# Kernel optimization log

Hardware: AMD Instinct MI355X
Metric: run time of the kernel (lower is better)

Reference implementation:

```python
import jax, jax.numpy as jnp
import numpy as np

NS = [65536, 16384, 4096, 1024, 256, 64]          # nodes per level (64 = 8 graphs x 8 dense voxels)
ES = [1048576, 262144, 65536, 16384, 4096]        # edges per level (avg degree 16)
INS = [1, 15, 23, 31, 39]
OUTS = [12, 20, 28, 36, 44]
K = 5                                             # kernel_size


def setup_inputs():
    keys = iter(jax.random.split(jax.random.key(0), 64))
    d = {'x': jax.random.normal(next(keys), (NS[0], 1), jnp.float32),
         'pos': jax.random.uniform(next(keys), (NS[0], 3), jnp.float32)}
    for l in range(5):
        n, e, ci, co = NS[l], ES[l], INS[l], OUTS[l]
        d[f'src{l}'] = jax.random.randint(next(keys), (e,), 0, n)
        d[f'dst{l}'] = jax.random.randint(next(keys), (e,), 0, n)
        d[f'eattr{l}'] = jax.random.normal(next(keys), (e, 3), jnp.float32)
        d[f'cluster{l}'] = jax.random.randint(next(keys), (n,), 0, NS[l + 1])
        d[f'w1_{l}'] = jax.random.normal(next(keys), (3, K), jnp.float32) * 0.5
        d[f'b1_{l}'] = jnp.zeros((K,), jnp.float32)
        d[f'w2_{l}'] = jax.random.normal(next(keys), (K, ci * co), jnp.float32) / np.float32(np.sqrt(K * ci))
        d[f'b2_{l}'] = jnp.zeros((ci * co,), jnp.float32)
        d[f'root_{l}'] = jax.random.normal(next(keys), (ci, co), jnp.float32) / np.float32(np.sqrt(ci))
        d[f'bias_{l}'] = jnp.zeros((co,), jnp.float32)
    d['fc_w'] = jax.random.normal(next(keys), (8 * 47, 10), jnp.float32) / np.float32(np.sqrt(8 * 47))
    d['fc_b'] = jnp.zeros((10,), jnp.float32)
    return d


def _conv(x, src, dst, eattr, w1, b1, w2, b2, root, bias, n):
    # edge-conditioned kernel: MLP(edge_attr) -> [E, ci, co]
    h = jnp.tanh(eattr @ w1 + b1)                                  # [E, K]
    We = (h @ w2 + b2).reshape(eattr.shape[0], x.shape[1], -1)     # [E, ci, co]
    msg = jnp.einsum('ei,eio->eo', x[src], We)                     # gather + per-edge matvec
    s = jax.ops.segment_sum(msg, dst, num_segments=n)
    cnt = jax.ops.segment_sum(jnp.ones((dst.shape[0], 1), x.dtype), dst, num_segments=n)
    agg = s / jnp.maximum(cnt, 1.0)                                # mean aggregation
    return agg + x @ root + bias, jnp.mean(jnp.square(We))


def _pool(x, pos, cluster, n_next):
    # sparse voxel max pool on features, mean on positions; pos concatenated to features
    xm = jax.ops.segment_max(x, cluster, num_segments=n_next)
    xm = jnp.where(jnp.isfinite(xm), xm, 0.0)                      # empty voxels -> 0
    ps = jax.ops.segment_sum(pos, cluster, num_segments=n_next)
    cnt = jax.ops.segment_sum(jnp.ones((pos.shape[0], 1), pos.dtype), cluster, num_segments=n_next)
    pm = ps / jnp.maximum(cnt, 1.0)
    return jnp.concatenate([xm, pm], axis=1), pm


def reference(x, pos, src0, dst0, eattr0, cluster0, w1_0, b1_0, w2_0, b2_0, root_0, bias_0,
              src1, dst1, eattr1, cluster1, w1_1, b1_1, w2_1, b2_1, root_1, bias_1,
              src2, dst2, eattr2, cluster2, w1_2, b1_2, w2_2, b2_2, root_2, bias_2,
              src3, dst3, eattr3, cluster3, w1_3, b1_3, w2_3, b2_3, root_3, bias_3,
              src4, dst4, eattr4, cluster4, w1_4, b1_4, w2_4, b2_4, root_4, bias_4,
              fc_w, fc_b):
    lv = [(src0, dst0, eattr0, cluster0, w1_0, b1_0, w2_0, b2_0, root_0, bias_0),
          (src1, dst1, eattr1, cluster1, w1_1, b1_1, w2_1, b2_1, root_1, bias_1),
          (src2, dst2, eattr2, cluster2, w1_2, b1_2, w2_2, b2_2, root_2, bias_2),
          (src3, dst3, eattr3, cluster3, w1_3, b1_3, w2_3, b2_3, root_3, bias_3),
          (src4, dst4, eattr4, cluster4, w1_4, b1_4, w2_4, b2_4, root_4, bias_4)]
    closs = jnp.float32(0.0)
    for l, (src, dst, ea, cl, w1, b1, w2, b2, rt, bs) in enumerate(lv):
        x, c = _conv(x, src, dst, ea, w1, b1, w2, b2, rt, bs, NS[l])
        closs = closs + c
        x, pos = _pool(x, pos, cl, NS[l + 1])
    feat = x.reshape(-1, 8 * 47)                                   # [B, 8*47]
    logits = feat @ fc_w + fc_b
    return jax.nn.log_softmax(logits, axis=1), closs
```

## Files before the change

kernel.cpp:

```cpp
#include <hip/hip_runtime.h>
#include <hip/hip_fp16.h>
#include <math.h>


#define NT0   512
#define TSZ0  2048
#define NBK0  256
#define CAP0  4608
#define NT1   128
#define TSZ1  2048
#define NBK1  256
#define CAP1  1280

__device__ __forceinline__ float ftanh(float x) {
    float e = __expf(2.f * x);
    return 1.f - 2.f / (e + 1.f);
}

__device__ __forceinline__ unsigned fenc(float f) {
    int b = __float_as_int(f);
    return (b < 0) ? ~(unsigned)b : ((unsigned)b | 0x80000000u);
}
__device__ __forceinline__ float fdec(unsigned u) {
    int b = (u & 0x80000000u) ? (int)(u & 0x7fffffffu) : ~(int)u;
    return __int_as_float(b);
}

__device__ __forceinline__ float row_val(const unsigned* __restrict__ row,
                                         int i, int CI) {
    float cn = __uint_as_float(row[CI]);
    if (i < CI - 3) return (cn == 0.f) ? 0.f : fdec(row[i]);
    return __uint_as_float(row[i]) / fmaxf(cn, 1.f);
}

struct Seg4 {
    const int* idx[4];
    int*       cnt[4];
    int*       rp [4];
    int*       out[4];
    int        n  [4];
    int        nb [4];
    int        tstart[5];
};

struct GA {
    const int *src0, *dst0; const float* ea0;
    const int *src1, *dst1; const float* ea1;
    const float *x0, *pos0;
    const int* cluster[5];
    const float *w1[5], *b1[5], *w2[5], *b2[5], *root[5], *bias[5];
    const int* srcE[3]; const float* eaE[3];
    const float *fc_w, *fc_b;
    int *bcnt, *bcnt1;
    float4 *pay2, *pay1, *rec1;
    float *y0, *xn0;
    unsigned* raw[5];
    float *H, *sq;
    int *bs1, *rp1;
    Seg4 sg;
    float* out;
    int hb0[4], hsB;
};

__global__ __launch_bounds__(256) void k1_fuseA(GA A)
{
    __shared__ float4 stg[TSZ0];
    __shared__ unsigned char bkb[TSZ0];
    __shared__ int hb_[256], gb_[256], ls_[256], cu_[256];

    int B = blockIdx.x, t = threadIdx.x;

    if (B < NT0) {
        hb_[t] = 0;
        __syncthreads();
        int base = B * TSZ0 + t;
        int dreg[8];
        #pragma unroll
        for (int k = 0; k < 8; k++) {
            dreg[k] = A.dst0[base + k * 256];
            atomicAdd(&hb_[dreg[k] >> 8], 1);
        }
        __syncthreads();
        int c = hb_[t];
        gb_[t] = c ? atomicAdd(&A.bcnt[t], c) : 0;
        ls_[t] = c;
        __syncthreads();
        for (int d = 1; d < 256; d <<= 1) {
            int u = (t >= d) ? ls_[t - d] : 0;
            __syncthreads();
            ls_[t] += u;
            __syncthreads();
        }
        int ex = ls_[t] - c;
        ls_[t] = ex;
        cu_[t] = ex;
        __syncthreads();

        float w1r[15], b1r[5];
        #pragma unroll
        for (int i = 0; i < 15; i++) w1r[i] = A.w1[0][i];
        #pragma unroll
        for (int i = 0; i < 5; i++)  b1r[i] = A.b1[0][i];
        float acc[20];
        #pragma unroll
        for (int i = 0; i < 20; i++) acc[i] = 0.f;
        #pragma unroll
        for (int k = 0; k < 8; k++) {
            int i = base + k * 256;
// ... 145 lines not shown
        for (int i = 0; i < 5; i++)  b1r[i] = b1p[i];
        float acc[20];
        #pragma unroll
        for (int i = 0; i < 20; i++) acc[i] = 0.f;
        int base = bloc * 256 * K + t;
        for (int it = 0; it < K; it++) {
            int e = base + it * 256;
            if (e < Ej) {
                float e0 = ea[e * 3], e1 = ea[e * 3 + 1], e2 = ea[e * 3 + 2];
                float h[5];
                #pragma unroll
                for (int q = 0; q < 5; q++)
                    h[q] = ftanh(e0 * w1r[q] + e1 * w1r[5 + q] + e2 * w1r[10 + q] + b1r[q]);
                int p = 5;
                #pragma unroll
                for (int q = 0; q < 5; q++) {
                    acc[q] += h[q];
                    #pragma unroll
                    for (int q2 = q; q2 < 5; q2++) acc[p++] += h[q] * h[q2];
                }
            }
        }
        float* red = (float*)hb_;
        int wid = t >> 6, lane = t & 63;
        #pragma unroll
        for (int v = 0; v < 20; v++) {
            float s = acc[v];
            #pragma unroll
            for (int o = 32; o; o >>= 1) s += __shfl_down(s, o);
            if (lane == 0) red[wid * 20 + v] = s;
        }
        __syncthreads();
        if (t < 20)
            atomicAdd(&A.H[(j + 2) * 20 + t],
                      red[t] + red[20 + t] + red[40 + t] + red[60 + t]);
        return;
    }
    B -= A.hsB;
    {
        int s = 0;
        while (s < 3 && B >= A.sg.tstart[s + 1]) s++;
        int i0 = (B - A.sg.tstart[s]) * 1024;
        const int* idx = A.sg.idx[s];
        int* cnt = A.sg.cnt[s];
        int n = A.sg.n[s];
        #pragma unroll
        for (int j = 0; j < 4; j++) {
            int i = i0 + j * 256 + t;
            if (i < n) atomicAdd(&cnt[idx[i]], 1);
        }
    }
}

__global__ __launch_bounds__(256) void k2_fuseB(GA A)
{
    __shared__ alignas(16) char poolc[34048];
    int B = blockIdx.x, t = threadIdx.x;

    if (B < NBK0) {
        float4* stg = (float4*)poolc;
        float*  Sx  = (float*)(poolc + 16384);
        unsigned char* key = (unsigned char*)(poolc + 23552);
        short* inv = (short*)(poolc + 24576);
        int* hist = (int*)(poolc + 26624);
        int* st   = (int*)(poolc + 27648);
        int* cur  = (int*)(poolc + 28672);
        float* wsm = (float*)(poolc + 29696);

        if (t < 60) wsm[t] = A.w2[0][t];
        else if (t >= 64  && t < 76)  wsm[60 + t - 64]  = A.b2[0][t - 64];
        else if (t >= 128 && t < 140) wsm[72 + t - 128] = A.root[0][t - 128];
        else if (t >= 192 && t < 204) wsm[84 + t - 192] = A.bias[0][t - 192];

        int n = A.bcnt[B];
        if (n > CAP0) n = CAP0;
        size_t base = (size_t)B * CAP0;
        float s0 = 0.f, s1 = 0.f, s2 = 0.f, s3 = 0.f, s4 = 0.f, s5 = 0.f, dg = 0.f;

        for (int c0 = 0; c0 < n; c0 += 1024) {
            int cn = min(1024, n - c0);
            hist[t] = 0;
            __syncthreads();
            #pragma unroll
            for (int k = 0; k < 4; k++) {
                int j = k * 256 + t;
                if (j < cn) {
                    float4 R = A.pay2[base + c0 + j];
                    stg[j] = R;
                    int rel = (int)(__float_as_uint(R.w) >> 16) & 255;
                    key[j] = (unsigned char)rel;
                    atomicAdd(&hist[rel], 1);
                }
            }
            __syncthreads();
            int h = hist[t];
            int acc = h;
            st[t] = acc;
            __syncthreads();
            for (int d = 1; d < 256; d <<= 1) {
                int u = (t >= d) ? st[t - d] : 0;
                __syncthreads();
                acc += u;
                st[t] = acc;
                __syncthreads();
            }
            int ex = acc - h;
            st[t] = ex;
            cur[t] = ex;
            __syncthreads();
            #pragma unroll
            for (int k = 0; k < 4; k++) {
                int j = k * 256 + t;
                if (j < cn) {
                    int p = atomicAdd(&cur[key[j]], 1);
                    inv[p] = (short)j;
                }
            }
            __syncthreads();
            for (int q = st[t]; q < cur[t]; q++) {
                float4 R = stg[inv[q]];
                union HU { float f; __half2 h2; } a01, a23;
                a01.f = R.y; a23.f = R.z;
                unsigned wbits = __float_as_uint(R.w);
                float xv = R.x;
                s0 += xv;
                s1 += __low2float(a01.h2)  * xv;
                s2 += __high2float(a01.h2) * xv;
                s3 += __low2float(a23.h2)  * xv;
                s4 += __high2float(a23.h2) * xv;
                s5 += __half2float(__ushort_as_half((unsigned short)(wbits & 0xffffu))) * xv;
                dg += 1.f;
            }
            __syncthreads();
        }
        Sx[t] = s0;        Sx[256 + t] = s1;  Sx[512 + t] = s2;
        Sx[768 + t] = s3;  Sx[1024 + t] = s4; Sx[1280 + t] = s5;
        Sx[1536 + t] = dg;
        __syncthreads();
        int v0 = B << 8;
        for (int u = t; u < 256 * 12; u += 256) {
            int rel = u / 12, o = u - rel * 12;
            float dgv = Sx[1536 + rel];
            float invd = 1.f / fmaxf(dgv, 1.f);
            float msg = wsm[60 + o] * Sx[rel] + wsm[o] * Sx[256 + rel] +
                        wsm[12 + o] * Sx[512 + rel] + wsm[24 + o] * Sx[768 + rel] +
                        wsm[36 + o] * Sx[1024 + rel] + wsm[48 + o] * Sx[1280 + rel];
            float xv = A.x0[v0 + rel];
            A.y0[(size_t)(v0 + rel) * 12 + o] =
                msg * invd + xv * wsm[72 + o] + wsm[84 + o];
        }
        return;
    }
    B -= NBK0;
    int* sc = (int*)poolc;
    if (B < 1) {
        int c = A.bcnt1[t];
        if (c > CAP1) c = CAP1;
        sc[t] = c;
        __syncthreads();
        for (int d = 1; d < 256; d <<= 1) {
            int u = (t >= d) ? sc[t - d] : 0;
            __syncthreads();
            sc[t] += u;
            __syncthreads();
        }
        A.bs1[t] = sc[t] - c;
        if (t == 255) { A.bs1[256] = sc[255]; A.rp1[16384] = sc[255]; }
        return;
    }
    B -= 1;
    if (B < 3) {
        int s = B;
        int nb = A.sg.nb[s];
        const int* cnt = A.sg.cnt[s];
        int* rp = A.sg.rp[s];
        int VPT = nb >> 8;
        int i0 = t * VPT;
        int sum = 0;
        for (int k = 0; k < VPT; k++) sum += cnt[i0 + k];
        int acc = sum;
        sc[t] = acc;
        __syncthreads();
        for (int d = 1; d < 256; d <<= 1) {
            int t2 = (t >= d) ? sc[t - d] : 0;
            __syncthreads();
            acc += t2;
            sc[t] = acc;
            __syncthreads();
        }
        int running = acc - sum;
        for (int k = 0; k < VPT; k++) {
            rp[i0 + k] = running;
            running += cnt[i0 + k];
        }
        if (t == 255) rp[nb] = running;
        return;
    }
    B -= 3;
    if (B < 1) {
        int* big = (int*)poolc;
        int* scx = (int*)(poolc + 32768);
        int* tot = (int*)(poolc + 33792);
        const int* cnt = A.sg.cnt[3];
        int* rp = A.sg.rp[3];
        int carry = 0;
        for (int p = 0; p < 2; p++) {
            if (p == 1) carry = tot[0];
// ... 48 lines not shown
            float w[5];
            #pragma unroll
            for (int k = 0; k < 5; k++) w[k] = w2l[k * cico + u];
            int p = 0;
            #pragma unroll
            for (int k = 0; k < 5; k++) {
                #pragma unroll
                for (int k2 = k; k2 < 5; k2++) d[p++] += w[k] * w[k2];
            }
            #pragma unroll
            for (int k = 0; k < 5; k++) d[15 + k] += b * w[k];
            d[20] += b * b;
        }
        #pragma unroll
        for (int i = 0; i < 21; i++) {
            #pragma unroll
            for (int off = 32; off; off >>= 1) d[i] += __shfl_down(d[i], off);
        }
        if (t == 0) {
            static const int EA[5] = {1048576, 262144, 65536, 16384, 4096};
            const float* H1 = A.H + l * 20;
            const float* H2 = H1 + 5;
            float sq = (float)EA[l] * d[20];
            #pragma unroll
            for (int k = 0; k < 5; k++) sq += 2.f * d[15 + k] * H1[k];
            int p = 0;
            #pragma unroll
            for (int k = 0; k < 5; k++) {
                #pragma unroll
                for (int k2 = k; k2 < 5; k2++) {
                    sq += ((k == k2) ? 1.f : 2.f) * d[p] * H2[p];
                    p++;
                }
            }
            A.sq[l] = sq;
        }
    }
}

__global__ __launch_bounds__(256) void k3_fuseC(GA A)
{
    __shared__ float4 st4[CAP1];
    __shared__ short  inv[CAP1];
    __shared__ int h64[64], l64[64], c64[64];
    int B = blockIdx.x, t = threadIdx.x;

    if (B < A.sg.tstart[4]) {
        int s = 0;
        while (s < 3 && B >= A.sg.tstart[s + 1]) s++;
        int i0 = (B - A.sg.tstart[s]) * 1024;
        const int* idx = A.sg.idx[s];
        int* cnt = A.sg.cnt[s];
        const int* rp = A.sg.rp[s];
        int* out = A.sg.out[s];
        int n = A.sg.n[s];
        #pragma unroll
        for (int j = 0; j < 4; j++) {
            int i = i0 + j * 256 + t;
            if (i < n) {
                int d = idx[i];
                int p = atomicSub(&cnt[d], 1) - 1;
                out[rp[d] + p] = i;
            }
        }
        return;
    }
    B -= A.sg.tstart[4];
    {
        int b = B;
        int n = A.bcnt1[b];
        if (n > CAP1) n = CAP1;
        size_t base = (size_t)b * CAP1;
        for (int j = t; j < n; j += 256) st4[j] = A.pay1[base + j];
        if (t < 64) h64[t] = 0;
        __syncthreads();
        for (int j = t; j < n; j += 256) {
            int rel = (int)(__float_as_uint(st4[j].x) >> 16) & 63;
            atomicAdd(&h64[rel], 1);
        }
        __syncthreads();
        if (t < 64) {
            int v = h64[t];
            int val = v;
            #pragma unroll
            for (int d = 1; d < 64; d <<= 1) {
                int u = __shfl_up(val, d);
                if (t >= d) val += u;
            }
            l64[t] = val - v;
            c64[t] = val - v;
        }
        __syncthreads();
        for (int j = t; j < n; j += 256) {
            int rel = (int)(__float_as_uint(st4[j].x) >> 16) & 63;
            int p = atomicAdd(&c64[rel], 1);
            inv[p] = (short)j;
        }
        __syncthreads();
        int lo = A.bs1[b];
        for (int j = t; j < n; j += 256)
            A.rec1[lo + j] = st4[inv[j]];
        if (t < 64) A.rp1[(b << 6) + t] = lo + l64[t];
    }
}

__global__ __launch_bounds__(256) void k4_pool0(GA A)
{
    int gt = blockIdx.x * 256 + threadIdx.x;
    if (gt >= 16384 * 15) return;
    int c = gt / 15, o = gt - c * 15;
    int r0 = A.sg.rp[3][c], r1 = A.sg.rp[3][c + 1];
    const int* cnid = A.sg.out[3];
    int d = r1 - r0;
    if (o < 12) {
        float m = -INFINITY;
        for (int j = r0; j < r1; j++)
            m = fmaxf(m, A.y0[(size_t)cnid[j] * 12 + o]);
        if (d == 0 || !isfinite(m)) m = 0.f;
        A.xn0[c * 15 + o] = m;
    } else {
        int k = o - 12;
        float sum = 0.f;
        for (int j = r0; j < r1; j++)
            sum += A.pos0[cnid[j] * 3 + k];
        A.xn0[c * 15 + o] = sum / fmaxf((float)d, 1.f);
    }
}

__global__ __launch_bounds__(256) void k5_conv1(GA A)
{
    constexpr int CI = 15, CO = 20, CH = 48, CICO = CI * CO, RN = 24;
    __shared__ float w1s[20];
    __shared__ float4 recb[CH];
    __shared__ int   svb[CH];
    __shared__ float hb[CH * 6];
    __shared__ float xs[CH * CI];
    __shared__ float Sx[6 * CI];
    __shared__ float xown[CI];

    int t = threadIdx.x, v = blockIdx.x;
    if (t < 20) w1s[t] = (t < 15) ? A.w1[1][t] : A.b1[1][t - 15];
    if (t < CI) xown[t] = A.xn0[v * CI + t];
    int r0 = A.rp1[v], r1 = A.rp1[v + 1];
    int d = r1 - r0;
    float acc = 0.f;

    for (int c0 = r0; c0 < r1; c0 += CH) {
        int cn = min(CH, r1 - c0);
        if (t < cn) {
            float4 R = A.rec1[c0 + t];
            recb[t] = R;
            svb[t]  = (int)(__float_as_uint(R.x) & 0xffffu);
            hb[t * 6] = 1.f;
        }
        __syncthreads();
        if (t < cn * 5) {
            int j = t / 5, k = t % 5;
            float e0 = recb[j].y, e1 = recb[j].z, e2 = recb[j].w;
            hb[j * 6 + 1 + k] =
                ftanh(e0 * w1s[k] + e1 * w1s[5 + k] + e2 * w1s[10 + k] + w1s[15 + k]);
        }
        for (int u = t; u < cn * CI; u += 256) {
            int j = u / CI, i = u - j * CI;
            xs[u] = A.xn0[svb[j] * CI + i];
        }
        __syncthreads();
        if (t < 6 * CI) {
            int i = t / 6, k6 = t - (t / 6) * 6;
            for (int j = 0; j < cn; j++)
                acc += hb[j * 6 + k6] * xs[j * CI + i];
        }
        __syncthreads();
    }

    if (t < 6 * CI) Sx[t] = acc;
    __syncthreads();

    if (t < CO) {
        float m = 0.f;
        const float* w2 = A.w2[1];
        const float* b2 = A.b2[1];
        for (int i = 0; i < CI; i++) {
            m += b2[i * CO + t] * Sx[i * 6];
            #pragma unroll
            for (int k = 0; k < 5; k++)
                m += w2[k * CICO + i * CO + t] * Sx[i * 6 + 1 + k];
        }
        m /= fmaxf((float)d, 1.f);
        for (int i = 0; i < CI; i++) m += xown[i] * A.root[1][i * CO + t];
        m += A.bias[1][t];
        int c = A.cluster[1][v];
        unsigned* orow = A.raw[1] + (size_t)c * RN;
        atomicMax(&orow[t], fenc(m));
        if (t < 3) atomicAdd((float*)&orow[CO + t], xown[CI - 3 + t]);
        if (t == 0) atomicAdd((float*)&orow[CO + 3], 1.f);
    }
}

template<int CI, int CO>
__global__ __launch_bounds__(256) void coopP_k(GA A, int l)
{
    constexpr int CH = 48, CICO = CI * CO, RL = CI + 1, RN = CO + 4;
    __shared__ float w1s[20];
    __shared__ int   eb[CH], svb[CH];
    __shared__ float hb[CH * 6];
    __shared__ float xs[CH * CI];
    __shared__ float Sx[6 * CI];
    __shared__ float xown[CI];

    int t = threadIdx.x, v = blockIdx.x;
    int s = l - 2;
    const unsigned* rin = A.raw[l - 1];
    const int* rp = A.sg.rp[s];
    const int* eid = A.sg.out[s];
    const int* src = A.srcE[s];
    const float* eattr = A.eaE[s];

    if (t < 20) w1s[t] = (t < 15) ? A.w1[l][t] : A.b1[l][t - 15];
    if (t < CI) xown[t] = row_val(rin + (size_t)v * RL, t, CI);
    int r0 = rp[v], r1 = rp[v + 1];
    int d = r1 - r0;
    float acc = 0.f;

    for (int c0 = r0; c0 < r1; c0 += CH) {
        int cn = min(CH, r1 - c0);
        if (t < cn) {
            int e = eid[c0 + t];
            eb[t]  = e;
            svb[t] = src[e];
            hb[t * 6] = 1.f;
        }
        __syncthreads();
        if (t < cn * 5) {
            int j = t / 5, k = t % 5;
            int e = eb[j];
            float e0 = eattr[e * 3], e1 = eattr[e * 3 + 1], e2 = eattr[e * 3 + 2];
            hb[j * 6 + 1 + k] =
                ftanh(e0 * w1s[k] + e1 * w1s[5 + k] + e2 * w1s[10 + k] + w1s[15 + k]);
        }
        for (int u = t; u < cn * CI; u += 256) {
            int j = u / CI, i = u - j * CI;
            xs[u] = row_val(rin + (size_t)svb[j] * RL, i, CI);
        }
        __syncthreads();
        if (t < 6 * CI) {
            int i = t / 6, k6 = t - (t / 6) * 6;
            for (int j = 0; j < cn; j++)
                acc += hb[j * 6 + k6] * xs[j * CI + i];
        }
        __syncthreads();
    }

    if (t < 6 * CI) Sx[t] = acc;
    __syncthreads();

    if (t < CO) {
        float m = 0.f;
        const float* w2 = A.w2[l];
        const float* b2 = A.b2[l];
        for (int i = 0; i < CI; i++) {
            m += b2[i * CO + t] * Sx[i * 6];
            #pragma unroll
            for (int k = 0; k < 5; k++)
                m += w2[k * CICO + i * CO + t] * Sx[i * 6 + 1 + k];
        }
        m /= fmaxf((float)d, 1.f);
        for (int i = 0; i < CI; i++) m += xown[i] * A.root[l][i * CO + t];
        m += A.bias[l][t];
        int c = A.cluster[l][v];
        unsigned* orow = A.raw[l] + (size_t)c * RN;
        atomicMax(&orow[t], fenc(m));
        if (t < 3) atomicAdd((float*)&orow[CO + t], xown[CI - 3 + t]);
        if (t == 0) atomicAdd((float*)&orow[CO + 3], 1.f);
    }
}

__global__ __launch_bounds__(128) void k9_fc(GA A)
{
    __shared__ float feat[8 * 376];
    __shared__ float logit[80];
    __shared__ float roff[8];
    const unsigned* r5 = A.raw[4];
    for (int idx = threadIdx.x; idx < 64 * 47; idx += 128) {
        int n = idx / 47, i = idx - n * 47;
        int b = n >> 3, s = n & 7;
        feat[b * 376 + s * 47 + i] = row_val(r5 + (size_t)n * 48, i, 47);
    }
    __syncthreads();
    int t = threadIdx.x;
    if (t < 80) {
        int b = t / 10, j = t % 10;
        float acc = A.fc_b[j];
        for (int k = 0; k < 376; k++) acc += feat[b * 376 + k] * A.fc_w[k * 10 + j];
        logit[t] = acc;
    }
    __syncthreads();
    if (t < 8) {
        float m = -1e30f;
        for (int j = 0; j < 10; j++) m = fmaxf(m, logit[t * 10 + j]);
        float ssum = 0.f;
        for (int j = 0; j < 10; j++) ssum += expf(logit[t * 10 + j] - m);
        roff[t] = m + logf(ssum);
    }
    __syncthreads();
    if (t < 80) A.out[t] = logit[t] - roff[t / 10];
    if (t == 0) {
        const float* sq = A.sq;
        float closs = 0.f;
        closs += sq[0] * (1.0f / 12582912.0f);
        closs += sq[1] * (1.0f / 78643200.0f);
        closs += sq[2] * (1.0f / 42205184.0f);
        closs += sq[3] * (1.0f / 18284544.0f);
        closs += sq[4] * (1.0f / 7028736.0f);
        A.out[80] = closs;
    }
}


extern "C" void kernel_launch(void* const* d_in, const int* in_sizes, int n_in,
                              void* d_out, int out_size, void* d_ws, size_t ws_size,
                              hipStream_t stream)
{
    static const int NSa[6] = {65536, 16384, 4096, 1024, 256, 64};
    static const int ESa[5] = {1048576, 262144, 65536, 16384, 4096};
    static const int RNa[5] = {16, 24, 32, 40, 48};

    int* wsw = (int*)d_ws;
    size_t off = 0;
    auto alw = [&](size_t n) -> size_t {
        size_t p = off; off += (n + 63) & ~(size_t)63; return p;
    };
    size_t degO[5];
    for (int l = 2; l < 5; l++) degO[l] = alw(NSa[l]);
    size_t cdeg0O = alw(NSa[1]);
    size_t HO    = alw(100);
    size_t bcO   = alw(NBK0);
    size_t bc1O  = alw(NBK1);
    size_t rawO[5];
    for (int l = 1; l < 5; l++) rawO[l] = alw((size_t)NSa[l + 1] * RNa[l]);
    size_t zeroWords = off;
    size_t rpO[5], eidO[5];
    for (int l = 2; l < 5; l++) rpO[l]  = alw(NSa[l] + 1);
    size_t crp0O = alw(NSa[1] + 1);
    for (int l = 2; l < 5; l++) eidO[l] = alw(ESa[l]);
    size_t cnid0O = alw(NSa[0]);
    size_t pay2O = alw((size_t)NBK0 * CAP0 * 4);
    size_t y0O   = alw((size_t)NSa[0] * 12);
    size_t xn0O  = alw((size_t)NSa[1] * 15);
    size_t bs1O  = alw(NBK1 + 1);
    size_t pay1O = alw((size_t)NBK1 * CAP1 * 4);
    size_t rec1O = alw((size_t)ESa[1] * 4);
    size_t rp1O  = alw(NSa[1] + 1);
    size_t sqO   = alw(8);

    GA A{};
    A.src0 = (const int*)d_in[2];  A.dst0 = (const int*)d_in[3];
    A.ea0  = (const float*)d_in[4];
    A.src1 = (const int*)d_in[12]; A.dst1 = (const int*)d_in[13];
    A.ea1  = (const float*)d_in[14];
    A.x0   = (const float*)d_in[0];
    A.pos0 = (const float*)d_in[1];
    for (int l = 0; l < 5; l++) {
        A.cluster[l] = (const int*)d_in[5 + 10 * l];
        A.w1[l]   = (const float*)d_in[6 + 10 * l];
        A.b1[l]   = (const float*)d_in[7 + 10 * l];
        A.w2[l]   = (const float*)d_in[8 + 10 * l];
        A.b2[l]   = (const float*)d_in[9 + 10 * l];
        A.root[l] = (const float*)d_in[10 + 10 * l];
        A.bias[l] = (const float*)d_in[11 + 10 * l];
    }
    for (int s = 0; s < 3; s++) {
        A.srcE[s] = (const int*)d_in[2 + 10 * (s + 2)];
        A.eaE[s]  = (const float*)d_in[4 + 10 * (s + 2)];
    }
    A.fc_w = (const float*)d_in[52];
    A.fc_b = (const float*)d_in[53];
    A.bcnt  = wsw + bcO;
    A.bcnt1 = wsw + bc1O;
    A.pay2 = (float4*)(wsw + pay2O);
    A.pay1 = (float4*)(wsw + pay1O);
    A.rec1 = (float4*)(wsw + rec1O);
    A.y0   = (float*)(wsw + y0O);
    A.xn0  = (float*)(wsw + xn0O);
    for (int l = 1; l < 5; l++) A.raw[l] = (unsigned*)(wsw + rawO[l]);
    A.H  = (float*)(wsw + HO);
    A.sq = (float*)(wsw + sqO);
    A.bs1 = wsw + bs1O;
    A.rp1 = wsw + rp1O;
    A.out = (float*)d_out;

    int tiles = 0;
    for (int s = 0; s < 3; s++) {
        int l = s + 2;
        A.sg.idx[s] = (const int*)d_in[3 + 10 * l];
        A.sg.cnt[s] = wsw + degO[l];
        A.sg.rp [s] = wsw + rpO[l];
        A.sg.out[s] = wsw + eidO[l];
        A.sg.n  [s] = ESa[l];
        A.sg.nb [s] = NSa[l];
        A.sg.tstart[s] = tiles;
        tiles += (ESa[l] + 1023) / 1024;
    }
    A.sg.idx[3] = (const int*)d_in[5];
    A.sg.cnt[3] = wsw + cdeg0O;
    A.sg.rp [3] = wsw + crp0O;
    A.sg.out[3] = wsw + cnid0O;
    A.sg.n  [3] = NSa[0];
    A.sg.nb [3] = NSa[1];
    A.sg.tstart[3] = tiles;
    tiles += (NSa[0] + 1023) / 1024;
    A.sg.tstart[4] = tiles;

    int hsB = 0;
    A.hb0[0] = 0;
    for (int j = 0; j < 3; j++) {
        hsB += (ESa[j + 2] + 2047) / 2048;
        A.hb0[j + 1] = hsB;
    }
    A.hsB = hsB;

    hipMemsetAsync(d_ws, 0, zeroWords * 4, stream);

    k1_fuseA<<<NT0 + NT1 + hsB + tiles, 256, 0, stream>>>(A);
    k2_fuseB<<<NBK0 + 1 + 3 + 1 + 5,    256, 0, stream>>>(A);
    k3_fuseC<<<tiles + NBK1,            256, 0, stream>>>(A);
    k4_pool0<<<(16384 * 15 + 255) / 256, 256, 0, stream>>>(A);
    k5_conv1<<<NSa[1],                  256, 0, stream>>>(A);
    coopP_k<23, 28><<<NSa[2],           256, 0, stream>>>(A, 2);
    coopP_k<31, 36><<<NSa[3],           256, 0, stream>>>(A, 3);
    coopP_k<39, 44><<<NSa[4],           256, 0, stream>>>(A, 4);
    k9_fc<<<1, 128, 0, stream>>>(A);
}
```

Measured before the change: 342.1 us.

## Write level-0 conv outputs in cluster-sorted order and shrink per-node conv blocks

Moves the level-0 conv out of the scan kernel into its own kernel that runs after the cluster counting sort. It writes y0 rows directly at each node's sorted cluster slot and stores positions in that same order, so the pooling kernel reads contiguous rows instead of gathering through a node-id list. It also cuts the per-node conv kernels for levels 1-4 from 256 to 64 threads, looping over the work, to reduce idle lanes. The cost is one extra launch and an extra positions copy.

```diff
diff --git a/kernel.cpp b/kernel.cpp
--- a/kernel.cpp
+++ b/kernel.cpp
@@ -54,6 +54,8 @@
     int *bcnt, *bcnt1;
     float4 *pay2, *pay1, *rec1;
     float *y0, *xn0;
+    int* rank0;
+    float* posp;
     unsigned* raw[5];
     float *H, *sq;
     int *bs1, *rp1;
@@ -305,107 +307,12 @@
     }
 }
 
-__global__ __launch_bounds__(256) void k2_fuseB(GA A)
+__global__ __launch_bounds__(256) void k2_scans(GA A)
 {
     __shared__ alignas(16) char poolc[34048];
     int B = blockIdx.x, t = threadIdx.x;
-
-    if (B < NBK0) {
-        float4* stg = (float4*)poolc;
-        float*  Sx  = (float*)(poolc + 16384);
-        unsigned char* key = (unsigned char*)(poolc + 23552);
-        short* inv = (short*)(poolc + 24576);
-        int* hist = (int*)(poolc + 26624);
-        int* st   = (int*)(poolc + 27648);
-        int* cur  = (int*)(poolc + 28672);
-        float* wsm = (float*)(poolc + 29696);
-
-        if (t < 60) wsm[t] = A.w2[0][t];
-        else if (t >= 64  && t < 76)  wsm[60 + t - 64]  = A.b2[0][t - 64];
-        else if (t >= 128 && t < 140) wsm[72 + t - 128] = A.root[0][t - 128];
-        else if (t >= 192 && t < 204) wsm[84 + t - 192] = A.bias[0][t - 192];
-
-        int n = A.bcnt[B];
-        if (n > CAP0) n = CAP0;
-        size_t base = (size_t)B * CAP0;
-        float s0 = 0.f, s1 = 0.f, s2 = 0.f, s3 = 0.f, s4 = 0.f, s5 = 0.f, dg = 0.f;
-
-        for (int c0 = 0; c0 < n; c0 += 1024) {
-            int cn = min(1024, n - c0);
-            hist[t] = 0;
-            __syncthreads();
-            #pragma unroll
-            for (int k = 0; k < 4; k++) {
-                int j = k * 256 + t;
-                if (j < cn) {
-                    float4 R = A.pay2[base + c0 + j];
-                    stg[j] = R;
-                    int rel = (int)(__float_as_uint(R.w) >> 16) & 255;
-                    key[j] = (unsigned char)rel;
-                    atomicAdd(&hist[rel], 1);
-                }
-            }
-            __syncthreads();
-            int h = hist[t];
-            int acc = h;
-            st[t] = acc;
-            __syncthreads();
-            for (int d = 1; d < 256; d <<= 1) {
-                int u = (t >= d) ? st[t - d] : 0;
-                __syncthreads();
-                acc += u;
-                st[t] = acc;
-                __syncthreads();
-            }
-            int ex = acc - h;
-            st[t] = ex;
-            cur[t] = ex;
-            __syncthreads();
-            #pragma unroll
-            for (int k = 0; k < 4; k++) {
-                int j = k * 256 + t;
-                if (j < cn) {
-                    int p = atomicAdd(&cur[key[j]], 1);
-                    inv[p] = (short)j;
-                }
-            }
-            __syncthreads();
-            for (int q = st[t]; q < cur[t]; q++) {
-                float4 R = stg[inv[q]];
-                union HU { float f; __half2 h2; } a01, a23;
-                a01.f = R.y; a23.f = R.z;
-                unsigned wbits = __float_as_uint(R.w);
-                float xv = R.x;
-                s0 += xv;
-                s1 += __low2float(a01.h2)  * xv;
-                s2 += __high2float(a01.h2) * xv;
-                s3 += __low2float(a23.h2)  * xv;
-                s4 += __high2float(a23.h2) * xv;
-                s5 += __half2float(__ushort_as_half((unsigned short)(wbits & 0xffffu))) * xv;
-                dg += 1.f;
-            }
-            __syncthreads();
-        }
-        Sx[t] = s0;        Sx[256 + t] = s1;  Sx[512 + t] = s2;
-        Sx[768 + t] = s3;  Sx[1024 + t] = s4; Sx[1280 + t] = s5;
-        Sx[1536 + t] = dg;
-        __syncthreads();
-        int v0 = B << 8;
-        for (int u = t; u < 256 * 12; u += 256) {
-            int rel = u / 12, o = u - rel * 12;
-            float dgv = Sx[1536 + rel];
-            float invd = 1.f / fmaxf(dgv, 1.f);
-            float msg = wsm[60 + o] * Sx[rel] + wsm[o] * Sx[256 + rel] +
-                        wsm[12 + o] * Sx[512 + rel] + wsm[24 + o] * Sx[768 + rel] +
-                        wsm[36 + o] * Sx[1024 + rel] + wsm[48 + o] * Sx[1280 + rel];
-            float xv = A.x0[v0 + rel];
-            A.y0[(size_t)(v0 + rel) * 12 + o] =
-                msg * invd + xv * wsm[72 + o] + wsm[84 + o];
-        }
-        return;
-    }
-    B -= NBK0;
     int* sc = (int*)poolc;
+
     if (B < 1) {
         int c = A.bcnt1[t];
         if (c > CAP1) c = CAP1;
@@ -560,15 +467,31 @@
         const int* idx = A.sg.idx[s];
         int* cnt = A.sg.cnt[s];
         const int* rp = A.sg.rp[s];
-        int* out = A.sg.out[s];
         int n = A.sg.n[s];
-        #pragma unroll
-        for (int j = 0; j < 4; j++) {
-            int i = i0 + j * 256 + t;
-            if (i < n) {
-                int d = idx[i];
-                int p = atomicSub(&cnt[d], 1) - 1;
-                out[rp[d] + p] = i;
+        if (s == 3) {
+            #pragma unroll
+            for (int j = 0; j < 4; j++) {
+                int i = i0 + j * 256 + t;
+                if (i < n) {
+                    int d = idx[i];
+                    int p = atomicSub(&cnt[d], 1) - 1;
+                    int slot = rp[d] + p;
+                    A.rank0[i] = slot;
+                    A.posp[(size_t)slot * 3]     = A.pos0[(size_t)i * 3];
+                    A.posp[(size_t)slot * 3 + 1] = A.pos0[(size_t)i * 3 + 1];
+                    A.posp[(size_t)slot * 3 + 2] = A.pos0[(size_t)i * 3 + 2];
+                }
+            }
+        } else {
+            int* out = A.sg.out[s];
+            #pragma unroll
+            for (int j = 0; j < 4; j++) {
+                int i = i0 + j * 256 + t;
+                if (i < n) {
+                    int d = idx[i];
+                    int p = atomicSub(&cnt[d], 1) - 1;
+                    out[rp[d] + p] = i;
+                }
             }
         }
         return;
@@ -612,30 +535,124 @@
     }
 }
 
-__global__ __launch_bounds__(256) void k4_pool0(GA A)
+__global__ __launch_bounds__(256) void k4_conv0c(GA A)
+{
+    __shared__ float4 stg[1024];
+    __shared__ float  Sx[7 * 256];
+    __shared__ unsigned char key[1024];
+    __shared__ short  inv[1024];
+    __shared__ int hist[256], st[256], cur[256], slotL[256];
+    __shared__ float wsm[96];
+    int B = blockIdx.x, t = threadIdx.x;
+
+    if (t < 60) wsm[t] = A.w2[0][t];
+    else if (t >= 64  && t < 76)  wsm[60 + t - 64]  = A.b2[0][t - 64];
+    else if (t >= 128 && t < 140) wsm[72 + t - 128] = A.root[0][t - 128];
+    else if (t >= 192 && t < 204) wsm[84 + t - 192] = A.bias[0][t - 192];
+    int v0 = B << 8;
+    slotL[t] = A.rank0[v0 + t];
+
+    int n = A.bcnt[B];
+    if (n > CAP0) n = CAP0;
+    size_t base = (size_t)B * CAP0;
+    float s0 = 0.f, s1 = 0.f, s2 = 0.f, s3 = 0.f, s4 = 0.f, s5 = 0.f, dg = 0.f;
+
+    for (int c0 = 0; c0 < n; c0 += 1024) {
+        int cn = min(1024, n - c0);
+        hist[t] = 0;
+        __syncthreads();
+        #pragma unroll
+        for (int k = 0; k < 4; k++) {
+            int j = k * 256 + t;
+            if (j < cn) {
+                float4 R = A.pay2[base + c0 + j];
+                stg[j] = R;
+                int rel = (int)(__float_as_uint(R.w) >> 16) & 255;
+                key[j] = (unsigned char)rel;
+                atomicAdd(&hist[rel], 1);
+            }
+        }
+        __syncthreads();
+        int h = hist[t];
+        int acc = h;
+        st[t] = acc;
+        __syncthreads();
+        for (int d = 1; d < 256; d <<= 1) {
+            int u = (t >= d) ? st[t - d] : 0;
+            __syncthreads();
+            acc += u;
+            st[t] = acc;
+            __syncthreads();
+        }
+        int ex = acc - h;
+        st[t] = ex;
+        cur[t] = ex;
+        __syncthreads();
+        #pragma unroll
+        for (int k = 0; k < 4; k++) {
+            int j = k * 256 + t;
+            if (j < cn) {
+                int p = atomicAdd(&cur[key[j]], 1);
+                inv[p] = (short)j;
+            }
+        }
+        __syncthreads();
+        for (int q = st[t]; q < cur[t]; q++) {
+            float4 R = stg[inv[q]];
+            union HU { float f; __half2 h2; } a01, a23;
+            a01.f = R.y; a23.f = R.z;
+            unsigned wbits = __float_as_uint(R.w);
+            float xv = R.x;
+            s0 += xv;
+            s1 += __low2float(a01.h2)  * xv;
+            s2 += __high2float(a01.h2) * xv;
+            s3 += __low2float(a23.h2)  * xv;
+            s4 += __high2float(a23.h2) * xv;
+            s5 += __half2float(__ushort_as_half((unsigned short)(wbits & 0xffffu))) * xv;
+            dg += 1.f;
+        }
+        __syncthreads();
+    }
+    Sx[t] = s0;        Sx[256 + t] = s1;  Sx[512 + t] = s2;
+    Sx[768 + t] = s3;  Sx[1024 + t] = s4; Sx[1280 + t] = s5;
+    Sx[1536 + t] = dg;
+    __syncthreads();
+    for (int u = t; u < 256 * 12; u += 256) {
+        int rel = u / 12, o = u - rel * 12;
+        float dgv = Sx[1536 + rel];
+        float invd = 1.f / fmaxf(dgv, 1.f);
+        float msg = wsm[60 + o] * Sx[rel] + wsm[o] * Sx[256 + rel] +
+                    wsm[12 + o] * Sx[512 + rel] + wsm[24 + o] * Sx[768 + rel] +
+                    wsm[36 + o] * Sx[1024 + rel] + wsm[48 + o] * Sx[1280 + rel];
+        float xv = A.x0[v0 + rel];
+        A.y0[(size_t)slotL[rel] * 12 + o] =
+            msg * invd + xv * wsm[72 + o] + wsm[84 + o];
+    }
+}
+
+__global__ __launch_bounds__(256) void k5_pool0(GA A)
 {
     int gt = blockIdx.x * 256 + threadIdx.x;
     if (gt >= 16384 * 15) return;
     int c = gt / 15, o = gt - c * 15;
     int r0 = A.sg.rp[3][c], r1 = A.sg.rp[3][c + 1];
-    const int* cnid = A.sg.out[3];
     int d = r1 - r0;
     if (o < 12) {
         float m = -INFINITY;
         for (int j = r0; j < r1; j++)
-            m = fmaxf(m, A.y0[(size_t)cnid[j] * 12 + o]);
+            m = fmaxf(m, A.y0[(size_t)j * 12 + o]);
         if (d == 0 || !isfinite(m)) m = 0.f;
         A.xn0[c * 15 + o] = m;
     } else {
         int k = o - 12;
         float sum = 0.f;
         for (int j = r0; j < r1; j++)
-            sum += A.pos0[cnid[j] * 3 + k];
+            sum += A.posp[(size_t)j * 3 + k];
         A.xn0[c * 15 + o] = sum / fmaxf((float)d, 1.f);
     }
 }
 
-__global__ __launch_bounds__(256) void k5_conv1(GA A)
+__global__ __launch_bounds__(64) void k6_conv1(GA A)
 {
     constexpr int CI = 15, CO = 20, CH = 48, CICO = CI * CO, RN = 24;
     __shared__ float w1s[20];
@@ -643,7 +660,7 @@
     __shared__ int   svb[CH];
     __shared__ float hb[CH * 6];
     __shared__ float xs[CH * CI];
-    __shared__ float Sx[6 * CI];
+    __shared__ float Sx[128];
     __shared__ float xown[CI];
 
     int t = threadIdx.x, v = blockIdx.x;
@@ -651,7 +668,7 @@
     if (t < CI) xown[t] = A.xn0[v * CI + t];
     int r0 = A.rp1[v], r1 = A.rp1[v + 1];
     int d = r1 - r0;
-    float acc = 0.f;
+    float a0 = 0.f, a1 = 0.f;
 
     for (int c0 = r0; c0 < r1; c0 += CH) {
         int cn = min(CH, r1 - c0);
@@ -662,26 +679,38 @@
             hb[t * 6] = 1.f;
         }
         __syncthreads();
-        if (t < cn * 5) {
-            int j = t / 5, k = t % 5;
+        for (int u = t; u < cn * 5; u += 64) {
+            int j = u / 5, k = u - j * 5;
             float e0 = recb[j].y, e1 = recb[j].z, e2 = recb[j].w;
             hb[j * 6 + 1 + k] =
                 ftanh(e0 * w1s[k] + e1 * w1s[5 + k] + e2 * w1s[10 + k] + w1s[15 + k]);
         }
-        for (int u = t; u < cn * CI; u += 256) {
+        for (int u = t; u < cn * CI; u += 64) {
             int j = u / CI, i = u - j * CI;
             xs[u] = A.xn0[svb[j] * CI + i];
         }
         __syncthreads();
-        if (t < 6 * CI) {
-            int i = t / 6, k6 = t - (t / 6) * 6;
-            for (int j = 0; j < cn; j++)
-                acc += hb[j * 6 + k6] * xs[j * CI + i];
-        }
-        __syncthreads();
-    }
-
-    if (t < 6 * CI) Sx[t] = acc;
+        {
+            int u = t;
+            if (u < 6 * CI) {
+                int i = u / 6, k6 = u - (u / 6) * 6;
+                float s = 0.f;
+                for (int j = 0; j < cn; j++) s += hb[j * 6 + k6] * xs[j * CI + i];
+                a0 += s;
+            }
+            u = t + 64;
+            if (u < 6 * CI) {
+                int i = u / 6, k6 = u - (u / 6) * 6;
+                float s = 0.f;
+                for (int j = 0; j < cn; j++) s += hb[j * 6 + k6] * xs[j * CI + i];
+                a1 += s;
+            }
+        }
+        __syncthreads();
+    }
+
+    if (t < 6 * CI) Sx[t] = a0;
+    if (t + 64 < 6 * CI) Sx[t + 64] = a1;
     __syncthreads();
 
     if (t < CO) {
@@ -706,14 +735,14 @@
 }
 
 template<int CI, int CO>
-__global__ __launch_bounds__(256) void coopP_k(GA A, int l)
+__global__ __launch_bounds__(64) void coopP_k(GA A, int l)
 {
     constexpr int CH = 48, CICO = CI * CO, RL = CI + 1, RN = CO + 4;
     __shared__ float w1s[20];
     __shared__ int   eb[CH], svb[CH];
     __shared__ float hb[CH * 6];
     __shared__ float xs[CH * CI];
-    __shared__ float Sx[6 * CI];
+    __shared__ float Sx[256];
     __shared__ float xown[CI];
 
     int t = threadIdx.x, v = blockIdx.x;
@@ -728,7 +757,7 @@
     if (t < CI) xown[t] = row_val(rin + (size_t)v * RL, t, CI);
     int r0 = rp[v], r1 = rp[v + 1];
     int d = r1 - r0;
-    float acc = 0.f;
+    float av[4] = {0.f, 0.f, 0.f, 0.f};
 
     for (int c0 = r0; c0 < r1; c0 += CH) {
         int cn = min(CH, r1 - c0);
@@ -739,27 +768,36 @@
             hb[t * 6] = 1.f;
         }
         __syncthreads();
-        if (t < cn * 5) {
-            int j = t / 5, k = t % 5;
+        for (int u = t; u < cn * 5; u += 64) {
+            int j = u / 5, k = u - j * 5;
             int e = eb[j];
             float e0 = eattr[e * 3], e1 = eattr[e * 3 + 1], e2 = eattr[e * 3 + 2];
             hb[j * 6 + 1 + k] =
                 ftanh(e0 * w1s[k] + e1 * w1s[5 + k] + e2 * w1s[10 + k] + w1s[15 + k]);
         }
-        for (int u = t; u < cn * CI; u += 256) {
+        for (int u = t; u < cn * CI; u += 64) {
             int j = u / CI, i = u - j * CI;
             xs[u] = row_val(rin + (size_t)svb[j] * RL, i, CI);
         }
         __syncthreads();
-        if (t < 6 * CI) {
-            int i = t / 6, k6 = t - (t / 6) * 6;
-            for (int j = 0; j < cn; j++)
-                acc += hb[j * 6 + k6] * xs[j * CI + i];
-        }
-        __syncthreads();
-    }
-
-    if (t < 6 * CI) Sx[t] = acc;
+        #pragma unroll
+        for (int r = 0; r < 4; r++) {
+            int u = t + r * 64;
+            if (u < 6 * CI) {
+                int i = u / 6, k6 = u - (u / 6) * 6;
+                float s2 = 0.f;
+                for (int j = 0; j < cn; j++) s2 += hb[j * 6 + k6] * xs[j * CI + i];
+                av[r] += s2;
+            }
+        }
+        __syncthreads();
+    }
+
+    #pragma unroll
+    for (int r = 0; r < 4; r++) {
+        int u = t + r * 64;
+        if (u < 6 * CI) Sx[u] = av[r];
+    }
     __syncthreads();
 
     if (t < CO) {
@@ -783,7 +821,7 @@
     }
 }
 
-__global__ __launch_bounds__(128) void k9_fc(GA A)
+__global__ __launch_bounds__(128) void k10_fc(GA A)
 {
     __shared__ float feat[8 * 376];
     __shared__ float logit[80];
@@ -851,7 +889,8 @@
     for (int l = 2; l < 5; l++) rpO[l]  = alw(NSa[l] + 1);
     size_t crp0O = alw(NSa[1] + 1);
     for (int l = 2; l < 5; l++) eidO[l] = alw(ESa[l]);
-    size_t cnid0O = alw(NSa[0]);
+    size_t rank0O = alw(NSa[0]);
+    size_t pospO  = alw((size_t)NSa[0] * 3);
     size_t pay2O = alw((size_t)NBK0 * CAP0 * 4);
     size_t y0O   = alw((size_t)NSa[0] * 12);
     size_t xn0O  = alw((size_t)NSa[1] * 15);
@@ -890,6 +929,8 @@
     A.rec1 = (float4*)(wsw + rec1O);
     A.y0   = (float*)(wsw + y0O);
     A.xn0  = (float*)(wsw + xn0O);
+    A.rank0 = wsw + rank0O;
+    A.posp  = (float*)(wsw + pospO);
     for (int l = 1; l < 5; l++) A.raw[l] = (unsigned*)(wsw + rawO[l]);
     A.H  = (float*)(wsw + HO);
     A.sq = (float*)(wsw + sqO);
@@ -912,7 +953,7 @@
     A.sg.idx[3] = (const int*)d_in[5];
     A.sg.cnt[3] = wsw + cdeg0O;
     A.sg.rp [3] = wsw + crp0O;
-    A.sg.out[3] = wsw + cnid0O;
+    A.sg.out[3] = wsw + rank0O;
     A.sg.n  [3] = NSa[0];
     A.sg.nb [3] = NSa[1];
     A.sg.tstart[3] = tiles;
@@ -930,12 +971,13 @@
     hipMemsetAsync(d_ws, 0, zeroWords * 4, stream);
 
     k1_fuseA<<<NT0 + NT1 + hsB + tiles, 256, 0, stream>>>(A);
-    k2_fuseB<<<NBK0 + 1 + 3 + 1 + 5,    256, 0, stream>>>(A);
+    k2_scans<<<1 + 3 + 1 + 5,           256, 0, stream>>>(A);
     k3_fuseC<<<tiles + NBK1,            256, 0, stream>>>(A);
-    k4_pool0<<<(16384 * 15 + 255) / 256, 256, 0, stream>>>(A);
-    k5_conv1<<<NSa[1],                  256, 0, stream>>>(A);
-    coopP_k<23, 28><<<NSa[2],           256, 0, stream>>>(A, 2);
-    coopP_k<31, 36><<<NSa[3],           256, 0, stream>>>(A, 3);
-    coopP_k<39, 44><<<NSa[4],           256, 0, stream>>>(A, 4);
-    k9_fc<<<1, 128, 0, stream>>>(A);
-}
+    k4_conv0c<<<NBK0,                   256, 0, stream>>>(A);
+    k5_pool0<<<(16384 * 15 + 255) / 256, 256, 0, stream>>>(A);
+    k6_conv1<<<NSa[1],                  64, 0, stream>>>(A);
+    coopP_k<23, 28><<<NSa[2],           64, 0, stream>>>(A, 2);
+    coopP_k<31, 36><<<NSa[3],           64, 0, stream>>>(A, 3);
+    coopP_k<39, 44><<<NSa[4],           64, 0, stream>>>(A, 4);
+    k10_fc<<<1, 128, 0, stream>>>(A);
+}
```

Result: slower. 360.4 us (+5.3%).

## Scatter level-0 conv output into cluster-sorted order for contiguous pooling

Applied to the files above, without the earlier changes.

The level-0 conv is moved out of the scan kernel into its own kernel that runs after the cluster counting-sort. The conv now writes each node's output row to its sorted slot, and positions are likewise permuted into sorted order. The pool kernel then reads y0 and positions contiguously instead of through an index indirection. This costs one extra kernel launch and removes the overlap of conv0 with the scan blocks, and it adds scattered writes.

```diff
diff --git a/kernel.cpp b/kernel.cpp
--- a/kernel.cpp
+++ b/kernel.cpp
@@ -54,6 +54,8 @@
     int *bcnt, *bcnt1;
     float4 *pay2, *pay1, *rec1;
     float *y0, *xn0;
+    int* rank0;
+    float* posp;
     unsigned* raw[5];
     float *H, *sq;
     int *bs1, *rp1;
@@ -305,107 +307,12 @@
     }
 }
 
-__global__ __launch_bounds__(256) void k2_fuseB(GA A)
+__global__ __launch_bounds__(256) void k2_scans(GA A)
 {
     __shared__ alignas(16) char poolc[34048];
     int B = blockIdx.x, t = threadIdx.x;
-
-    if (B < NBK0) {
-        float4* stg = (float4*)poolc;
-        float*  Sx  = (float*)(poolc + 16384);
-        unsigned char* key = (unsigned char*)(poolc + 23552);
-        short* inv = (short*)(poolc + 24576);
-        int* hist = (int*)(poolc + 26624);
-        int* st   = (int*)(poolc + 27648);
-        int* cur  = (int*)(poolc + 28672);
-        float* wsm = (float*)(poolc + 29696);
-
-        if (t < 60) wsm[t] = A.w2[0][t];
-        else if (t >= 64  && t < 76)  wsm[60 + t - 64]  = A.b2[0][t - 64];
-        else if (t >= 128 && t < 140) wsm[72 + t - 128] = A.root[0][t - 128];
-        else if (t >= 192 && t < 204) wsm[84 + t - 192] = A.bias[0][t - 192];
-
-        int n = A.bcnt[B];
-        if (n > CAP0) n = CAP0;
-        size_t base = (size_t)B * CAP0;
-        float s0 = 0.f, s1 = 0.f, s2 = 0.f, s3 = 0.f, s4 = 0.f, s5 = 0.f, dg = 0.f;
-
-        for (int c0 = 0; c0 < n; c0 += 1024) {
-            int cn = min(1024, n - c0);
-            hist[t] = 0;
-            __syncthreads();
-            #pragma unroll
-            for (int k = 0; k < 4; k++) {
-                int j = k * 256 + t;
-                if (j < cn) {
-                    float4 R = A.pay2[base + c0 + j];
-                    stg[j] = R;
-                    int rel = (int)(__float_as_uint(R.w) >> 16) & 255;
-                    key[j] = (unsigned char)rel;
-                    atomicAdd(&hist[rel], 1);
-                }
-            }
-            __syncthreads();
-            int h = hist[t];
-            int acc = h;
-            st[t] = acc;
-            __syncthreads();
-            for (int d = 1; d < 256; d <<= 1) {
-                int u = (t >= d) ? st[t - d] : 0;
-                __syncthreads();
-                acc += u;
-                st[t] = acc;
-                __syncthreads();
-            }
-            int ex = acc - h;
-            st[t] = ex;
-            cur[t] = ex;
-            __syncthreads();
-            #pragma unroll
-            for (int k = 0; k < 4; k++) {
-                int j = k * 256 + t;
-                if (j < cn) {
-                    int p = atomicAdd(&cur[key[j]], 1);
-                    inv[p] = (short)j;
-                }
-            }
-            __syncthreads();
-            for (int q = st[t]; q < cur[t]; q++) {
-                float4 R = stg[inv[q]];
-                union HU { float f; __half2 h2; } a01, a23;
-                a01.f = R.y; a23.f = R.z;
-                unsigned wbits = __float_as_uint(R.w);
-                float xv = R.x;
-                s0 += xv;
-                s1 += __low2float(a01.h2)  * xv;
-                s2 += __high2float(a01.h2) * xv;
-                s3 += __low2float(a23.h2)  * xv;
-                s4 += __high2float(a23.h2) * xv;
-                s5 += __half2float(__ushort_as_half((unsigned short)(wbits & 0xffffu))) * xv;
-                dg += 1.f;
-            }
-            __syncthreads();
-        }
-        Sx[t] = s0;        Sx[256 + t] = s1;  Sx[512 + t] = s2;
-        Sx[768 + t] = s3;  Sx[1024 + t] = s4; Sx[1280 + t] = s5;
-        Sx[1536 + t] = dg;
-        __syncthreads();
-        int v0 = B << 8;
-        for (int u = t; u < 256 * 12; u += 256) {
-            int rel = u / 12, o = u - rel * 12;
-            float dgv = Sx[1536 + rel];
-            float invd = 1.f / fmaxf(dgv, 1.f);
-            float msg = wsm[60 + o] * Sx[rel] + wsm[o] * Sx[256 + rel] +
-                        wsm[12 + o] * Sx[512 + rel] + wsm[24 + o] * Sx[768 + rel] +
-                        wsm[36 + o] * Sx[1024 + rel] + wsm[48 + o] * Sx[1280 + rel];
-            float xv = A.x0[v0 + rel];
-            A.y0[(size_t)(v0 + rel) * 12 + o] =
-                msg * invd + xv * wsm[72 + o] + wsm[84 + o];
-        }
-        return;
-    }
-    B -= NBK0;
     int* sc = (int*)poolc;
+
     if (B < 1) {
         int c = A.bcnt1[t];
         if (c > CAP1) c = CAP1;
@@ -560,15 +467,31 @@
         const int* idx = A.sg.idx[s];
         int* cnt = A.sg.cnt[s];
         const int* rp = A.sg.rp[s];
-        int* out = A.sg.out[s];
         int n = A.sg.n[s];
-        #pragma unroll
-        for (int j = 0; j < 4; j++) {
-            int i = i0 + j * 256 + t;
-            if (i < n) {
-                int d = idx[i];
-                int p = atomicSub(&cnt[d], 1) - 1;
-                out[rp[d] + p] = i;
+        if (s == 3) {
+            #pragma unroll
+            for (int j = 0; j < 4; j++) {
+                int i = i0 + j * 256 + t;
+                if (i < n) {
+                    int d = idx[i];
+                    int p = atomicSub(&cnt[d], 1) - 1;
+                    int slot = rp[d] + p;
+                    A.rank0[i] = slot;
+                    A.posp[(size_t)slot * 3]     = A.pos0[(size_t)i * 3];
+                    A.posp[(size_t)slot * 3 + 1] = A.pos0[(size_t)i * 3 + 1];
+                    A.posp[(size_t)slot * 3 + 2] = A.pos0[(size_t)i * 3 + 2];
+                }
+            }
+        } else {
+            int* out = A.sg.out[s];
+            #pragma unroll
+            for (int j = 0; j < 4; j++) {
+                int i = i0 + j * 256 + t;
+                if (i < n) {
+                    int d = idx[i];
+                    int p = atomicSub(&cnt[d], 1) - 1;
+                    out[rp[d] + p] = i;
+                }
             }
         }
         return;
@@ -612,30 +535,124 @@
     }
 }
 
-__global__ __launch_bounds__(256) void k4_pool0(GA A)
+__global__ __launch_bounds__(256) void k4_conv0c(GA A)
+{
+    __shared__ float4 stg[1024];
+    __shared__ float  Sx[7 * 256];
+    __shared__ unsigned char key[1024];
+    __shared__ short  inv[1024];
+    __shared__ int hist[256], st[256], cur[256], slotL[256];
+    __shared__ float wsm[96];
+    int B = blockIdx.x, t = threadIdx.x;
+
+    if (t < 60) wsm[t] = A.w2[0][t];
+    else if (t >= 64  && t < 76)  wsm[60 + t - 64]  = A.b2[0][t - 64];
+    else if (t >= 128 && t < 140) wsm[72 + t - 128] = A.root[0][t - 128];
+    else if (t >= 192 && t < 204) wsm[84 + t - 192] = A.bias[0][t - 192];
+    int v0 = B << 8;
+    slotL[t] = A.rank0[v0 + t];
+
+    int n = A.bcnt[B];
+    if (n > CAP0) n = CAP0;
+    size_t base = (size_t)B * CAP0;
+    float s0 = 0.f, s1 = 0.f, s2 = 0.f, s3 = 0.f, s4 = 0.f, s5 = 0.f, dg = 0.f;
+
+    for (int c0 = 0; c0 < n; c0 += 1024) {
+        int cn = min(1024, n - c0);
+        hist[t] = 0;
+        __syncthreads();
+        #pragma unroll
+        for (int k = 0; k < 4; k++) {
+            int j = k * 256 + t;
+            if (j < cn) {
+                float4 R = A.pay2[base + c0 + j];
+                stg[j] = R;
+                int rel = (int)(__float_as_uint(R.w) >> 16) & 255;
+                key[j] = (unsigned char)rel;
+                atomicAdd(&hist[rel], 1);
+            }
+        }
+        __syncthreads();
+        int h = hist[t];
+        int acc = h;
+        st[t] = acc;
+        __syncthreads();
+        for (int d = 1; d < 256; d <<= 1) {
+            int u = (t >= d) ? st[t - d] : 0;
+            __syncthreads();
+            acc += u;
+            st[t] = acc;
+            __syncthreads();
+        }
+        int ex = acc - h;
+        st[t] = ex;
+        cur[t] = ex;
+        __syncthreads();
+        #pragma unroll
+        for (int k = 0; k < 4; k++) {
+            int j = k * 256 + t;
+            if (j < cn) {
+                int p = atomicAdd(&cur[key[j]], 1);
+                inv[p] = (short)j;
+            }
+        }
+        __syncthreads();
+        for (int q = st[t]; q < cur[t]; q++) {
+            float4 R = stg[inv[q]];
+            union HU { float f; __half2 h2; } a01, a23;
+            a01.f = R.y; a23.f = R.z;
+            unsigned wbits = __float_as_uint(R.w);
+            float xv = R.x;
+            s0 += xv;
+            s1 += __low2float(a01.h2)  * xv;
+            s2 += __high2float(a01.h2) * xv;
+            s3 += __low2float(a23.h2)  * xv;
+            s4 += __high2float(a23.h2) * xv;
+            s5 += __half2float(__ushort_as_half((unsigned short)(wbits & 0xffffu))) * xv;
+            dg += 1.f;
+        }
+        __syncthreads();
+    }
+    Sx[t] = s0;        Sx[256 + t] = s1;  Sx[512 + t] = s2;
+    Sx[768 + t] = s3;  Sx[1024 + t] = s4; Sx[1280 + t] = s5;
+    Sx[1536 + t] = dg;
+    __syncthreads();
+    for (int u = t; u < 256 * 12; u += 256) {
+        int rel = u / 12, o = u - rel * 12;
+        float dgv = Sx[1536 + rel];
+        float invd = 1.f / fmaxf(dgv, 1.f);
+        float msg = wsm[60 + o] * Sx[rel] + wsm[o] * Sx[256 + rel] +
+                    wsm[12 + o] * Sx[512 + rel] + wsm[24 + o] * Sx[768 + rel] +
+                    wsm[36 + o] * Sx[1024 + rel] + wsm[48 + o] * Sx[1280 + rel];
+        float xv = A.x0[v0 + rel];
+        A.y0[(size_t)slotL[rel] * 12 + o] =
+            msg * invd + xv * wsm[72 + o] + wsm[84 + o];
+    }
+}
+
+__global__ __launch_bounds__(256) void k5_pool0(GA A)
 {
     int gt = blockIdx.x * 256 + threadIdx.x;
     if (gt >= 16384 * 15) return;
     int c = gt / 15, o = gt - c * 15;
     int r0 = A.sg.rp[3][c], r1 = A.sg.rp[3][c + 1];
-    const int* cnid = A.sg.out[3];
     int d = r1 - r0;
     if (o < 12) {
         float m = -INFINITY;
         for (int j = r0; j < r1; j++)
-            m = fmaxf(m, A.y0[(size_t)cnid[j] * 12 + o]);
+            m = fmaxf(m, A.y0[(size_t)j * 12 + o]);
         if (d == 0 || !isfinite(m)) m = 0.f;
         A.xn0[c * 15 + o] = m;
     } else {
         int k = o - 12;
         float sum = 0.f;
         for (int j = r0; j < r1; j++)
-            sum += A.pos0[cnid[j] * 3 + k];
+            sum += A.posp[(size_t)j * 3 + k];
         A.xn0[c * 15 + o] = sum / fmaxf((float)d, 1.f);
     }
 }
 
-__global__ __launch_bounds__(256) void k5_conv1(GA A)
+__global__ __launch_bounds__(256) void k6_conv1(GA A)
 {
     constexpr int CI = 15, CO = 20, CH = 48, CICO = CI * CO, RN = 24;
     __shared__ float w1s[20];
@@ -783,7 +800,7 @@
     }
 }
 
-__global__ __launch_bounds__(128) void k9_fc(GA A)
+__global__ __launch_bounds__(128) void k10_fc(GA A)
 {
     __shared__ float feat[8 * 376];
     __shared__ float logit[80];
@@ -851,7 +868,8 @@
     for (int l = 2; l < 5; l++) rpO[l]  = alw(NSa[l] + 1);
     size_t crp0O = alw(NSa[1] + 1);
     for (int l = 2; l < 5; l++) eidO[l] = alw(ESa[l]);
-    size_t cnid0O = alw(NSa[0]);
+    size_t rank0O = alw(NSa[0]);
+    size_t pospO  = alw((size_t)NSa[0] * 3);
     size_t pay2O = alw((size_t)NBK0 * CAP0 * 4);
     size_t y0O   = alw((size_t)NSa[0] * 12);
     size_t xn0O  = alw((size_t)NSa[1] * 15);
@@ -890,6 +908,8 @@
     A.rec1 = (float4*)(wsw + rec1O);
     A.y0   = (float*)(wsw + y0O);
     A.xn0  = (float*)(wsw + xn0O);
+    A.rank0 = wsw + rank0O;
+    A.posp  = (float*)(wsw + pospO);
     for (int l = 1; l < 5; l++) A.raw[l] = (unsigned*)(wsw + rawO[l]);
     A.H  = (float*)(wsw + HO);
     A.sq = (float*)(wsw + sqO);
@@ -912,7 +932,7 @@
     A.sg.idx[3] = (const int*)d_in[5];
     A.sg.cnt[3] = wsw + cdeg0O;
     A.sg.rp [3] = wsw + crp0O;
-    A.sg.out[3] = wsw + cnid0O;
+    A.sg.out[3] = wsw + rank0O;
     A.sg.n  [3] = NSa[0];
     A.sg.nb [3] = NSa[1];
     A.sg.tstart[3] = tiles;
@@ -930,12 +950,13 @@
     hipMemsetAsync(d_ws, 0, zeroWords * 4, stream);
 
     k1_fuseA<<<NT0 + NT1 + hsB + tiles, 256, 0, stream>>>(A);
-    k2_fuseB<<<NBK0 + 1 + 3 + 1 + 5,    256, 0, stream>>>(A);
+    k2_scans<<<1 + 3 + 1 + 5,           256, 0, stream>>>(A);
     k3_fuseC<<<tiles + NBK1,            256, 0, stream>>>(A);
-    k4_pool0<<<(16384 * 15 + 255) / 256, 256, 0, stream>>>(A);
-    k5_conv1<<<NSa[1],                  256, 0, stream>>>(A);
+    k4_conv0c<<<NBK0,                   256, 0, stream>>>(A);
+    k5_pool0<<<(16384 * 15 + 255) / 256, 256, 0, stream>>>(A);
+    k6_conv1<<<NSa[1],                  256, 0, stream>>>(A);
     coopP_k<23, 28><<<NSa[2],           256, 0, stream>>>(A, 2);
     coopP_k<31, 36><<<NSa[3],           256, 0, stream>>>(A, 3);
     coopP_k<39, 44><<<NSa[4],           256, 0, stream>>>(A, 4);
-    k9_fc<<<1, 128, 0, stream>>>(A);
-}
+    k10_fc<<<1, 128, 0, stream>>>(A);
+}
```

Result: slower. 350.9 us (+2.6%).
